# Performance work log

Hardware: AMD Instinct MI355X
Metric: run time of the kernel (lower is better)

Reference implementation:

```python
import jax, jax.numpy as jnp
import numpy as np

N, E = 50000, 800000
IN_CH, HID, OUT_CH = 128, 256, 40
L, R = 3, 16
EPS = 1e-12


def setup_inputs() -> dict:
    key = jax.random.key(0)
    ks = jax.random.split(key, 16)
    s = 0.05
    return {
        'x': jax.random.normal(ks[0], (N, IN_CH), jnp.float32),
        'edge_index': jax.random.randint(ks[1], (2, E), 0, N, dtype=jnp.int64),
        'W_in': jax.random.normal(ks[2], (IN_CH, HID), jnp.float32) * s,
        'b_in': jnp.zeros((HID,), jnp.float32),
        'centers': jax.random.normal(ks[3], (L, R, HID), jnp.float32),
        'log_sigma': jnp.zeros((L, R, HID), jnp.float32),
        'W_rule': jax.random.normal(ks[4], (L, R, HID, HID), jnp.float32) * s,
        'b_rule': jnp.zeros((L, R, HID), jnp.float32),
        'W_self': jax.random.normal(ks[5], (L, HID, HID), jnp.float32) * s,
        'b_self': jnp.zeros((L, HID), jnp.float32),
        'gamma': jnp.ones((L, HID), jnp.float32),
        'beta': jnp.zeros((L, HID), jnp.float32),
        'W_h1': jax.random.normal(ks[6], (HID, HID // 2), jnp.float32) * s,
        'b_h1': jnp.zeros((HID // 2,), jnp.float32),
        'W_h2': jax.random.normal(ks[7], (HID // 2, OUT_CH), jnp.float32) * s,
        'b_h2': jnp.zeros((OUT_CH,), jnp.float32),
    }


def membership(h, c, log_s):
    # Gaussian rule firing, expanded to matmuls to avoid [N,R,H] distance tensor
    inv_s2 = jnp.exp(-2.0 * log_s)                         # [R,H]
    d = (h * h) @ inv_s2.T - 2.0 * (h @ (c * inv_s2).T) \
        + jnp.sum(c * c * inv_s2, axis=-1)                 # [N,R]
    firing = jnp.exp(-0.5 * d)
    return firing / (jnp.sum(firing, axis=-1, keepdims=True) + EPS)


def fmpl(h, src, dst, c, log_s, W_r, b_r, W_s, b_s):
    n = h.shape[0]
    deg = jax.ops.segment_sum(jnp.ones(src.shape[0], h.dtype), dst, num_segments=n)
    agg = jax.ops.segment_sum(h[src], dst, num_segments=n) / jnp.clip(deg, 1.0)[:, None]
    mu = membership(h, c, log_s)                           # [N,R]
    per_rule = jnp.einsum('ni,rio->nro', agg, W_r) + b_r[None]  # [N,R,H]
    fuzzy = jnp.einsum('nr,nro->no', mu, per_rule)
    return h @ W_s + b_s + fuzzy


def batchnorm(x, g, b, eps=1e-5):
    m = jnp.mean(x, axis=0)
    v = jnp.var(x, axis=0)
    return (x - m) * jax.lax.rsqrt(v + eps) * g + b


def reference(x, edge_index, W_in, b_in, centers, log_sigma, W_rule, b_rule,
              W_self, b_self, gamma, beta, W_h1, b_h1, W_h2, b_h2):
    src, dst = edge_index[0], edge_index[1]
    h = jax.nn.relu(x @ W_in + b_in)                       # dropout = identity (eval)
    for l in range(L):
        h_new = fmpl(h, src, dst, centers[l], log_sigma[l], W_rule[l], b_rule[l],
                     W_self[l], b_self[l])
        h_new = jax.nn.relu(batchnorm(h_new, gamma[l], beta[l]))
        h = h + h_new
    logits = jax.nn.relu(h @ W_h1 + b_h1) @ W_h2 + b_h2
    return jax.nn.softmax(logits, axis=-1)
```

## Files before the change

kernel.cpp:

```cpp
#include <hip/hip_runtime.h>
#include <hip/hip_fp16.h>
#include <cstdint>
#include <cstddef>

using u16 = unsigned short;
using u32 = unsigned int;

typedef _Float16 half8 __attribute__((ext_vector_type(8)));
typedef float f32x4 __attribute__((ext_vector_type(4)));

static inline int cdiv(int a, int b) { return (a + b - 1) / b; }


__global__ void prep_k(const float* __restrict__ Wr,
                       const float* __restrict__ Ws, const float* __restrict__ br,
                       const float* __restrict__ W_in, const float* __restrict__ W_h1,
                       const float* __restrict__ W_h2,
                       const float* __restrict__ centers, const float* __restrict__ logsig,
                       u16* __restrict__ wcat,
                       u16* __restrict__ winp, u16* __restrict__ wh1p,
                       u16* __restrict__ wh2p,
                       u16* __restrict__ pcB, float* __restrict__ pccc,
                       int* __restrict__ zerobase, int nzero,
                       int Z, int Wb) {
    const int bid = blockIdx.x;
    const int tid = threadIdx.x;
    if (bid < Z) {
        int i = bid * 256 + tid;
        if (i < nzero) zerobase[i] = 0;
        return;
    }
    if (bid < Z + Wb) {
        size_t t = (size_t)(bid - Z) * 256 + tid;
        const size_t PL = 552u * 256u * 8u;
        int l = (int)(t / PL);
        size_t rem = t - (size_t)l * PL;
        int kp = (int)(rem >> 11);
        int o = (int)((rem >> 3) & 255);
        int e = (int)(rem & 7);
        int k = kp * 8 + e;
        float v;
        if (k < 4096)      v = Wr[((((size_t)l * 16 + (k >> 8)) * 256) + (k & 255)) * 256 + o];
        else if (k < 4352) v = Ws[(((size_t)l * 256) + (k - 4096)) * 256 + o];
        else if (k < 4368) v = br[(((size_t)l * 16) + (k - 4352)) * 256 + o];
        else               v = 0.f;
        union { u16 u; _Float16 h; } c; c.h = (_Float16)v;
        wcat[t] = c.u;
        return;
    }
    if (bid < Z + Wb + 128) {
        size_t t = (size_t)(bid - Z - Wb) * 256 + tid;
        int e = (int)(t & 7), o = (int)((t >> 3) & 255);
        int kp = (int)(t >> 11);
        union { u16 u; _Float16 h; } c; c.h = (_Float16)W_in[(size_t)(kp * 8 + e) * 256 + o];
        winp[t] = c.u;
        return;
    }
    if (bid < Z + Wb + 256) {
        size_t t = (size_t)(bid - Z - Wb - 128) * 256 + tid;
        int e = (int)(t & 7), o = (int)((t >> 3) & 127);
        int kp = (int)(t >> 10);
        union { u16 u; _Float16 h; } c; c.h = (_Float16)W_h1[(size_t)(kp * 8 + e) * 128 + o];
        wh1p[t] = c.u;
        return;
    }
    if (bid < Z + Wb + 256 + 24) {
        int t = (bid - Z - Wb - 256) * 256 + tid;
        int e = t & 7, col = (t >> 3) % 48, p = t / 384;
        int k = p * 8 + e;
        float v = (col < 40) ? W_h2[(size_t)k * 40 + col] : 0.f;
        union { u16 u; _Float16 h; } c; c.h = (_Float16)v;
        wh2p[t] = c.u;
        return;
    }
    {
        int lr = bid - (Z + Wb + 256 + 24);
        size_t idx = (size_t)lr * 256 + tid;
        float ls = logsig[idx];
        float inv = expf(-2.f * ls);
        float c = centers[idx];
        union { u16 u; _Float16 h; } c1, c2;
        c1.h = (_Float16)inv;
        c2.h = (_Float16)(-2.f * c * inv);
        pcB[(size_t)lr * 512 + tid] = c1.u;
        pcB[(size_t)lr * 512 + 256 + tid] = c2.u;
        __shared__ float sm[256];
        sm[tid] = c * c * inv;
        __syncthreads();
        for (int s = 128; s > 0; s >>= 1) { if (tid < s) sm[tid] += sm[tid + s]; __syncthreads(); }
        if (tid == 0) pccc[lr] = sm[0];
    }
}


__launch_bounds__(256, 4)
__global__ void csr_agg_g(const int* __restrict__ src, const int* __restrict__ dst,
                          int* __restrict__ deg, int* __restrict__ indptr,
                          int* __restrict__ cursor, float* __restrict__ deginv,
                          int* __restrict__ ssrc, int* __restrict__ csrctr,
                          const int* __restrict__ bflag, int* __restrict__ done,
                          const u16* __restrict__ h16, u16* __restrict__ agg16,
                          int E, int n) {
    if (bflag[511] == 0) return;
    const int tid = threadIdx.x;
    if (*done == 0) {
        auto gbar = [&](int id) {
            __threadfence();
            __syncthreads();
            if (tid == 0) {
                atomicAdd(csrctr, 1);
                while (atomicAdd(csrctr, 0) < 256 * id) __builtin_amdgcn_s_sleep(2);
            }
            __syncthreads();
        };
        for (int e = blockIdx.x * 256 + tid; e < E; e += 256 * 256)
            atomicAdd(&deg[dst[e]], 1);
        gbar(1);
        if (blockIdx.x == 0) {
            const int chunk = (n + 255) >> 8;
            int s0 = tid * chunk, s1 = s0 + chunk; if (s1 > n) s1 = n; if (s0 > n) s0 = n;
            int tot = 0;
            for (int i = s0; i < s1; ++i) tot += atomicAdd(&deg[i], 0);
            __shared__ int sm[256];
            sm[tid] = tot; __syncthreads();
            for (int off = 1; off < 256; off <<= 1) {
                int t = (tid >= off) ? sm[tid - off] : 0;
                __syncthreads(); sm[tid] += t; __syncthreads();
            }
            int base = sm[tid] - tot;
            for (int i = s0; i < s1; ++i) {
                int d = atomicAdd(&deg[i], 0);
                indptr[i] = base; cursor[i] = base;
                deginv[i] = 1.f / (float)(d > 1 ? d : 1);
                base += d;
            }
            if (tid == 255) indptr[n] = sm[255];
        }
        gbar(2);
        for (int e = blockIdx.x * 256 + tid; e < E; e += 256 * 256) {
            int d = dst[e];
            int pos = atomicAdd(&cursor[d], 1);
            ssrc[pos] = src[e];
        }
        gbar(3);
        if (blockIdx.x == 0 && tid == 0) *done = 1;
    }
    int lane = tid & 63, wave = tid >> 6;
    for (int node = blockIdx.x * 4 + wave; node < n; node += 256 * 4) {
        if (bflag[node >> 7] == 0) continue;
        int j0 = indptr[node], j1 = indptr[node + 1];
        float a0 = 0, a1 = 0, a2 = 0, a3 = 0;
        for (int j = j0; j < j1; ++j) {
            int sN = ssrc[j];
            union { uint2 u; _Float16 h[4]; } hv;
            hv.u = *(const uint2*)(h16 + (size_t)sN * 256 + lane * 4);
            a0 += (float)hv.h[0]; a1 += (float)hv.h[1];
            a2 += (float)hv.h[2]; a3 += (float)hv.h[3];
        }
        float di = deginv[node];
        union { uint2 u; _Float16 h[4]; } o;
        o.h[0] = (_Float16)(a0 * di); o.h[1] = (_Float16)(a1 * di);
        o.h[2] = (_Float16)(a2 * di); o.h[3] = (_Float16)(a3 * di);
        *(uint2*)(agg16 + (size_t)node * 256 + lane * 4) = o.u;
    }
}


__launch_bounds__(256)
__global__ void memb_k(const u16* __restrict__ h16, const u16* __restrict__ pcB,
                       const float* __restrict__ pccc,
                       u16* __restrict__ mu16, int* __restrict__ bflag, int n) {
    const int lane = threadIdx.x & 63, wave = threadIdx.x >> 6;
    const int q = lane >> 4, mm = lane & 15;
    const int n0 = (blockIdx.x * 4 + wave) * 16;
    if (n0 >= n) return;
    int nodeA = n0 + mm; if (nodeA >= n) nodeA = n - 1;
    const u16* hrow = h16 + (size_t)nodeA * 256;
    const u16* brow = pcB + (size_t)mm * 512;
    f32x4 acc = (f32x4){0.f, 0.f, 0.f, 0.f};
#pragma unroll
    for (int it = 0; it < 16; ++it) {
        int k = it * 32 + q * 8;
        half8 b = *(const half8*)(brow + k);
        half8 a;
        if (k < 256) {
            a = *(const half8*)(hrow + k);
            a = a * a;
        } else {
            a = *(const half8*)(hrow + (k - 256));
        }
        acc = __builtin_amdgcn_mfma_f32_16x16x32_f16(a, b, acc, 0, 0, 0);
    }
    float cc = pccc[mm];
    bool any = false;
#pragma unroll
    for (int r = 0; r < 4; ++r) {
        float d = acc[r] + cc;
        float f = expf(-0.5f * d);
        float s = f;
        s += __shfl_xor(s, 1); s += __shfl_xor(s, 2);
        s += __shfl_xor(s, 4); s += __shfl_xor(s, 8);
        int node = n0 + q * 4 + r;
        if (node < n) {
            union { u16 u; _Float16 h; } c2;
            c2.h = (_Float16)(f / (s + 1e-12f));
            mu16[(size_t)node * 16 + mm] = c2.u;
            if (c2.u != 0) any = true;
        }
    }
    if (__any(any) && lane == 0) {
        atomicOr(&bflag[n0 >> 7], 1);
        atomicOr(&bflag[511], 1);
    }
}


template <int MODE, int NCHUNK>
__launch_bounds__(256, 4)
__global__ void gemm_k(const u16* __restrict__ A, const u16* __restrict__ A2,
                       const u16* __restrict__ MU, const u16* __restrict__ Bp,
                       const float* __restrict__ bias, const int* __restrict__ bflag,
                       u16* __restrict__ outH, float* __restrict__ partial,
                       const u16* __restrict__ wh2, const float* __restrict__ bh2,
                       float* __restrict__ outF,
                       int nrows, int mcols, int astride) {
    __shared__ __align__(16) u16 lds[17408];
    __shared__ float bnbuf[512];
    u16* lA = lds;
    u16* lB = lds + 8192;
    const int tid = threadIdx.x;
    const int row0 = blockIdx.x * 128;
    const int c0 = blockIdx.y * 128;
    const int lane = tid & 63;
    const int q = lane >> 4, mm = lane & 15;
    const int wave = tid >> 6;
    const int wm = wave >> 1, wn = wave & 1;

    f32x4 acc[4][4];
#pragma unroll
    for (int i = 0; i < 4; ++i)
#pragma unroll
        for (int j = 0; j < 4; ++j) acc[i][j] = (f32x4){0.f, 0.f, 0.f, 0.f};

    int cb = 0, cbEnd = NCHUNK;
    if (MODE == 1 && bflag[blockIdx.x] == 0) { cb = 64; cbEnd = 68; }

    for (; cb < cbEnd; ++cb) {
#pragma unroll
        for (int it = 0; it < 4; ++it) {
            int idx = it * 256 + tid;
            int p = idx >> 7, col = idx & 127;
            uint4 v = *(const uint4*)(Bp + (((size_t)(cb * 8 + p)) * mcols + c0 + col) * 8);
            *(uint4*)(lB + (size_t)idx * 8) = v;
        }
#pragma unroll
        for (int it = 0; it < 4; ++it) {
            int idx = it * 256 + tid;
            int p = idx >> 7, row = idx & 127;
            int grow = row0 + row; if (grow >= nrows) grow = nrows - 1;
            uint4 v;
            if (MODE == 0) {
                const float* xr = (const float*)A + (size_t)grow * 128 + cb * 64 + (p << 3);
                float4 f0 = *(const float4*)xr;
                float4 f1 = *(const float4*)(xr + 4);
                union { uint4 u4; _Float16 h[8]; } cv;
                cv.h[0] = (_Float16)f0.x; cv.h[1] = (_Float16)f0.y;
                cv.h[2] = (_Float16)f0.z; cv.h[3] = (_Float16)f0.w;
                cv.h[4] = (_Float16)f1.x; cv.h[5] = (_Float16)f1.y;
                cv.h[6] = (_Float16)f1.z; cv.h[7] = (_Float16)f1.w;
                v = cv.u4;
            } else if (MODE == 2) {
                v = *(const uint4*)(A + (size_t)grow * astride + cb * 64 + p * 8);
            } else {
                if (cb < 64) {
                    int r = cb >> 2;
                    int i0 = ((cb & 3) << 6) + (p << 3);
                    v = *(const uint4*)(A + (size_t)grow * 256 + i0);
                    union { u16 u; _Float16 h; } mu; mu.u = MU[(size_t)grow * 16 + r];
                    union { uint4 u4; _Float16 h[8]; } wv; wv.u4 = v;
#pragma unroll
                    for (int j = 0; j < 8; ++j) wv.h[j] = wv.h[j] * mu.h;
                    v = wv.u4;
                } else if (cb < 68) {
                    int i0 = ((cb - 64) << 6) + (p << 3);
                    v = *(const uint4*)(A2 + (size_t)grow * 256 + i0);
                } else {
                    int j0 = p << 3;
                    if (j0 < 16) v = *(const uint4*)(MU + (size_t)grow * 16 + j0);
                    else v = (uint4){0, 0, 0, 0};
                }
            }
            *(uint4*)(lA + (size_t)idx * 8) = v;
        }
        __syncthreads();
#pragma unroll
        for (int kc = 0; kc < 2; ++kc) {
            int pp = kc * 4 + q;
            half8 af[4], bf[4];
#pragma unroll
            for (int mt = 0; mt < 4; ++mt)
                af[mt] = *(const half8*)(lA + ((size_t)pp * 128 + wm * 64 + mt * 16 + mm) * 8);
#pragma unroll
            for (int nt = 0; nt < 4; ++nt)
                bf[nt] = *(const half8*)(lB + ((size_t)pp * 128 + wn * 64 + nt * 16 + mm) * 8);
#pragma unroll
            for (int mt = 0; mt < 4; ++mt)
#pragma unroll
                for (int nt = 0; nt < 4; ++nt)
                    acc[mt][nt] = __builtin_amdgcn_mfma_f32_16x16x32_f16(af[mt], bf[nt], acc[mt][nt], 0, 0, 0);
        }
        __syncthreads();
    }

#pragma unroll
    for (int nt = 0; nt < 4; ++nt) {
        const int cl = wn * 64 + nt * 16 + mm;
        const int gcol = c0 + cl;
        float s = 0.f, ss = 0.f;
#pragma unroll
        for (int mt = 0; mt < 4; ++mt) {
#pragma unroll
            for (int r = 0; r < 4; ++r) {
                int row = wm * 64 + mt * 16 + q * 4 + r;
                float v = acc[mt][nt][r] + bias[gcol];
                if (MODE != 1) v = fmaxf(v, 0.f);
                union { u16 u; _Float16 h; } cc; cc.h = (_Float16)v;
                lds[row * 136 + cl] = cc.u;
                if (MODE == 1 && row0 + row < nrows) { s += v; ss += v * v; }
            }
        }
        if (MODE == 1) {
            s += __shfl_xor(s, 16);  s += __shfl_xor(s, 32);
            ss += __shfl_xor(ss, 16); ss += __shfl_xor(ss, 32);
            if (q == 0) {
                bnbuf[(wm * 128 + cl) * 2 + 0] = s;
                bnbuf[(wm * 128 + cl) * 2 + 1] = ss;
            }
        }
    }
    __syncthreads();

    if (MODE != 2) {
        int nr = nrows - row0; if (nr > 128) nr = 128;
#pragma unroll
        for (int it = 0; it < 8; ++it) {
            int idx = it * 256 + tid;
            int row = idx >> 4, cp = idx & 15;
            if (row < nr) {
                uint4 v = *(const uint4*)(lds + row * 136 + cp * 8);
                *(uint4*)(outH + (size_t)(row0 + row) * mcols + c0 + cp * 8) = v;
            }
        }
        if (MODE == 1) {
            int cl2 = tid >> 1, comp = tid & 1;
            float v = bnbuf[cl2 * 2 + comp] + bnbuf[(128 + cl2) * 2 + comp];
            partial[(size_t)blockIdx.x * 512 + comp * 256 + c0 + cl2] = v;
        }
    } else {
        const bool c2ok = (mm < 8);
        float b0 = bh2[mm], b1 = bh2[16 + mm];
        float b2 = c2ok ? bh2[32 + mm] : 0.f;
#pragma unroll
        for (int half = 0; half < 2; ++half) {
            int rbase = half * 64 + wave * 16;
            f32x4 hacc[3];
#pragma unroll
            for (int t = 0; t < 3; ++t) hacc[t] = (f32x4){0.f, 0.f, 0.f, 0.f};
#pragma unroll
            for (int c = 0; c < 4; ++c) {
                half8 a = *(const half8*)(lds + (rbase + mm) * 136 + c * 32 + q * 8);
#pragma unroll
                for (int t = 0; t < 3; ++t) {
                    half8 b = *(const half8*)(wh2 + ((size_t)(c * 4 + q) * 48 + t * 16 + mm) * 8);
                    hacc[t] = __builtin_amdgcn_mfma_f32_16x16x32_f16(a, b, hacc[t], 0, 0, 0);
                }
            }
#pragma unroll
            for (int r = 0; r < 4; ++r) {
                int node = row0 + rbase + q * 4 + r;
                float v0 = hacc[0][r] + b0;
                float v1 = hacc[1][r] + b1;
                float v2 = c2ok ? (hacc[2][r] + b2) : -3e38f;
                float m = fmaxf(fmaxf(v0, v1), v2);
                m = fmaxf(m, __shfl_xor(m, 1)); m = fmaxf(m, __shfl_xor(m, 2));
                m = fmaxf(m, __shfl_xor(m, 4)); m = fmaxf(m, __shfl_xor(m, 8));
                float e0 = expf(v0 - m), e1 = expf(v1 - m);
                float e2 = c2ok ? expf(v2 - m) : 0.f;
                float s = e0 + e1 + e2;
                s += __shfl_xor(s, 1); s += __shfl_xor(s, 2);
                s += __shfl_xor(s, 4); s += __shfl_xor(s, 8);
                float is = 1.f / s;
                if (node < nrows) {
                    float* op = outF + (size_t)node * 40;
                    op[mm] = e0 * is;
                    op[16 + mm] = e1 * is;
                    if (c2ok) op[32 + mm] = e2 * is;
                }
            }
        }
    }
}


__global__ void bnred_k(const float* __restrict__ partial, float* __restrict__ bnsum,
                        const float* __restrict__ gamma, const float* __restrict__ beta,
                        float* __restrict__ ab, int* __restrict__ bnctr, int n, int gx) {
    const int tid = threadIdx.x;
    const int g = blockIdx.x;
    float s = 0.f, qq = 0.f;
    for (int r = g; r < gx; r += 16) {
        s  += partial[(size_t)r * 512 + tid];
        qq += partial[(size_t)r * 512 + 256 + tid];
    }
    atomicAdd(&bnsum[tid], s);
    atomicAdd(&bnsum[256 + tid], qq);
    __threadfence();
    __shared__ int last;
    if (tid == 0) last = (atomicAdd(bnctr, 1) == 15);
    __syncthreads();
    if (!last) return;
    float su = atomicAdd(&bnsum[tid], 0.f);
    float sq = atomicAdd(&bnsum[256 + tid], 0.f);
    float invn = 1.f / (float)n;
    float m = su * invn;
    float al = gamma[tid] * rsqrtf(sq * invn - m * m + 1e-5f);
    ab[tid] = al;
    ab[256 + tid] = beta[tid] - m * al;
}


template <int DOMEMB>
__launch_bounds__(256)
__global__ void updmemb_k(const u16* __restrict__ pre16, const float* __restrict__ ab,
                          u16* __restrict__ h16,
                          const u16* __restrict__ pcB, const float* __restrict__ pccc,
                          u16* __restrict__ mu16, int* __restrict__ bflag, int n) {
    const int tid = threadIdx.x;
    const int lane = tid & 63, wave = tid >> 6;
    const int q = lane >> 4, mm = lane & 15;
    const int n0 = (blockIdx.x * 4 + wave) * 16;
    if (n0 >= n) return;
    const int node = n0 + mm;
    const bool valid = node < n;
    const int nodeC = valid ? node : n - 1;
    const size_t base = (size_t)nodeC * 256 + q * 8;

    half8 v16[8];
#pragma unroll
    for (int b = 0; b < 8; ++b) {
        int c = b * 32 + q * 8;
        float4 alA = *(const float4*)(ab + c);
        float4 alB = *(const float4*)(ab + c + 4);
        float4 shA = *(const float4*)(ab + 256 + c);
        float4 shB = *(const float4*)(ab + 256 + c + 4);
        float aarr[8] = {alA.x, alA.y, alA.z, alA.w, alB.x, alB.y, alB.z, alB.w};
        float harr[8] = {shA.x, shA.y, shA.z, shA.w, shB.x, shB.y, shB.z, shB.w};
        union { uint4 u; _Float16 hh[8]; } p, hv, o;
        p.u  = *(const uint4*)(pre16 + base + b * 32);
        hv.u = *(const uint4*)(h16 + base + b * 32);
#pragma unroll
        for (int j = 0; j < 8; ++j) {
            float v = (float)hv.hh[j] + fmaxf((float)p.hh[j] * aarr[j] + harr[j], 0.f);
            o.hh[j] = (_Float16)v;
        }
        if (valid) *(uint4*)(h16 + base + b * 32) = o.u;
        v16[b] = *(half8*)&o;
    }

    if (DOMEMB) {
        const u16* brow = pcB + (size_t)mm * 512;
        f32x4 acc = (f32x4){0.f, 0.f, 0.f, 0.f};
#pragma unroll
        for (int it = 0; it < 16; ++it) {
            half8 a = v16[it & 7];
            if (it < 8) a = a * a;
            half8 bb = *(const half8*)(brow + it * 32 + q * 8);
            acc = __builtin_amdgcn_mfma_f32_16x16x32_f16(a, bb, acc, 0, 0, 0);
        }
        float cc = pccc[mm];
        bool any = false;
#pragma unroll
        for (int r = 0; r < 4; ++r) {
            float d = acc[r] + cc;
            float f = expf(-0.5f * d);
            float s = f;
            s += __shfl_xor(s, 1); s += __shfl_xor(s, 2);
            s += __shfl_xor(s, 4); s += __shfl_xor(s, 8);
            int nd = n0 + q * 4 + r;
            if (nd < n) {
                union { u16 u; _Float16 h; } c2;
                c2.h = (_Float16)(f / (s + 1e-12f));
                mu16[(size_t)nd * 16 + mm] = c2.u;
                if (c2.u != 0) any = true;
            }
        }
        if (__any(any) && lane == 0) {
            atomicOr(&bflag[n0 >> 7], 1);
            atomicOr(&bflag[511], 1);
        }
    }
}


extern "C" void kernel_launch(void* const* d_in, const int* in_sizes, int n_in,
                              void* d_out, int out_size, void* d_ws, size_t ws_size,
                              hipStream_t stream) {
    const float* x       = (const float*)d_in[0];
    const int*   ei      = (const int*)d_in[1];
    const float* W_in    = (const float*)d_in[2];
    const float* b_in    = (const float*)d_in[3];
    const float* centers = (const float*)d_in[4];
    const float* logsig  = (const float*)d_in[5];
    const float* W_rule  = (const float*)d_in[6];
    const float* b_rule  = (const float*)d_in[7];
    const float* W_self  = (const float*)d_in[8];
    const float* b_self  = (const float*)d_in[9];
    const float* gamma   = (const float*)d_in[10];
    const float* beta    = (const float*)d_in[11];
    const float* W_h1    = (const float*)d_in[12];
    const float* b_h1    = (const float*)d_in[13];
    const float* W_h2    = (const float*)d_in[14];
    const float* b_h2    = (const float*)d_in[15];

    const int N = in_sizes[0] / 128;
    const int E = in_sizes[1] / 2;
    const int* e_src = ei;
    const int* e_dst = ei + E;

    char* w = (char*)d_ws;
    size_t off = 0;
    auto alloc = [&](size_t bytes) -> void* {
        void* p = w + off;
        off = (off + bytes + 255) & ~(size_t)255;
        return p;
    };

    const int gx = cdiv(N, 128);

    u16*   h16    = (u16*)  alloc((size_t)N * 256 * 2);
    u16*   pre16  = (u16*)  alloc((size_t)N * 256 * 2);
    u16*   agg16  = (u16*)  alloc((size_t)N * 256 * 2);
    u16*   mu16   = (u16*)  alloc((size_t)N * 16 * 2);
    u16*   wcat   = (u16*)  alloc((size_t)3 * 552 * 256 * 8 * 2);
    u16*   winp   = (u16*)  alloc((size_t)16 * 256 * 8 * 2);
    u16*   wh1p   = (u16*)  alloc((size_t)32 * 128 * 8 * 2);
    u16*   wh2p   = (u16*)  alloc((size_t)16 * 48 * 8 * 2);
    u16*   pcB    = (u16*)  alloc((size_t)48 * 512 * 2);
    float* pccc   = (float*)alloc((size_t)48 * 4);
    int*   indptr = (int*)  alloc((size_t)(N + 1) * 4);
    int*   cursor = (int*)  alloc((size_t)N * 4);
    float* deginv = (float*)alloc((size_t)N * 4);
    int*   ssrc   = (int*)  alloc((size_t)E * 4);
    float* partial= (float*)alloc((size_t)gx * 512 * 4);
    float* abA    = (float*)alloc((size_t)3 * 512 * 4);
    const int nzero = N + 3 * 512 + 3 * 512 + 16;
    int*   zerob  = (int*)  alloc((size_t)nzero * 4);
    int*   deg    = zerob;
    int*   bflagA = zerob + N;
    float* bnsumA = (float*)(zerob + N + 3 * 512);
    int*   misc   = zerob + N + 3 * 512 + 3 * 512;
    int*   done   = misc;
    int*   csrctr = misc + 1;
    int*   bnctr  = misc + 2;

    const int Z = cdiv(nzero, 256);
    const int Wb = 3 * 552 * 256 * 8 / 256;
    const int prep_grid = Z + Wb + 128 + 128 + 24 + 48;

    prep_k<<<prep_grid, 256, 0, stream>>>(W_rule, W_self, b_rule, W_in, W_h1, W_h2,
                                          centers, logsig, wcat, winp, wh1p, wh2p,
                                          pcB, pccc, zerob, nzero, Z, Wb);

    gemm_k<0, 2><<<dim3(gx, 2), 256, 0, stream>>>((const u16*)x, nullptr, nullptr, winp,
                                                  b_in, nullptr, h16, nullptr, nullptr,
                                                  nullptr, nullptr, N, 256, 128);
    memb_k<<<cdiv(N, 64), 256, 0, stream>>>(h16, pcB, pccc, mu16, bflagA, N);

    for (int l = 0; l < 3; ++l) {
        int* bf = bflagA + l * 512;
        float* bns = bnsumA + l * 512;
        float* ab = abA + l * 512;
        csr_agg_g<<<256, 256, 0, stream>>>(e_src, e_dst, deg, indptr, cursor, deginv,
                                           ssrc, csrctr, bf, done, h16, agg16, E, N);
        gemm_k<1, 69><<<dim3(gx, 2), 256, 0, stream>>>(agg16, h16, mu16,
                                                       wcat + (size_t)l * 552 * 256 * 8,
                                                       b_self + l * 256, bf, pre16,
                                                       partial, nullptr, nullptr, nullptr,
                                                       N, 256, 0);
        bnred_k<<<16, 256, 0, stream>>>(partial, bns, gamma + l * 256, beta + l * 256,
                                        ab, bnctr + l, N, gx);
        if (l < 2) {
            updmemb_k<1><<<cdiv(N, 64), 256, 0, stream>>>(pre16, ab, h16,
                                                          pcB + (size_t)(l + 1) * 16 * 512,
                                                          pccc + (l + 1) * 16, mu16,
                                                          bflagA + (l + 1) * 512, N);
        } else {
            updmemb_k<0><<<cdiv(N, 64), 256, 0, stream>>>(pre16, ab, h16,
                                                          nullptr, nullptr, nullptr,
                                                          nullptr, N);
        }
    }

    gemm_k<2, 4><<<dim3(gx, 1), 256, 0, stream>>>(h16, nullptr, nullptr, wh1p, b_h1,
                                                  nullptr, nullptr, nullptr, wh2p, b_h2,
                                                  (float*)d_out, N, 128, 256);
}
```

Baseline: 337.1 us.

## Use full-width GEMM tiles, fuse membership into input GEMM and drop BN reduction kernel

The main GEMM now computes all 256 output columns per 128-row block instead of splitting columns across two blocks. Each block loads the A tile (the mu-scaled aggregation) once rather than twice, at the cost of more accumulator registers and lower occupancy (launch bounds 2). The input GEMM also computes the first-layer membership in its epilogue, which removes the separate memb_k launch and a re-read of h. The batchnorm column sums are atomically accumulated directly from the GEMM, and alpha/shift are recomputed in updmemb_k, which eliminates the bnred_k launch. The head GEMM is split into its own kernel.

```diff
diff --git a/kernel.cpp b/kernel.cpp
--- a/kernel.cpp
+++ b/kernel.cpp
@@ -166,91 +166,40 @@
 }
 
 
-__launch_bounds__(256)
-__global__ void memb_k(const u16* __restrict__ h16, const u16* __restrict__ pcB,
-                       const float* __restrict__ pccc,
-                       u16* __restrict__ mu16, int* __restrict__ bflag, int n) {
-    const int lane = threadIdx.x & 63, wave = threadIdx.x >> 6;
-    const int q = lane >> 4, mm = lane & 15;
-    const int n0 = (blockIdx.x * 4 + wave) * 16;
-    if (n0 >= n) return;
-    int nodeA = n0 + mm; if (nodeA >= n) nodeA = n - 1;
-    const u16* hrow = h16 + (size_t)nodeA * 256;
-    const u16* brow = pcB + (size_t)mm * 512;
-    f32x4 acc = (f32x4){0.f, 0.f, 0.f, 0.f};
-#pragma unroll
-    for (int it = 0; it < 16; ++it) {
-        int k = it * 32 + q * 8;
-        half8 b = *(const half8*)(brow + k);
-        half8 a;
-        if (k < 256) {
-            a = *(const half8*)(hrow + k);
-            a = a * a;
-        } else {
-            a = *(const half8*)(hrow + (k - 256));
-        }
-        acc = __builtin_amdgcn_mfma_f32_16x16x32_f16(a, b, acc, 0, 0, 0);
-    }
-    float cc = pccc[mm];
-    bool any = false;
-#pragma unroll
-    for (int r = 0; r < 4; ++r) {
-        float d = acc[r] + cc;
-        float f = expf(-0.5f * d);
-        float s = f;
-        s += __shfl_xor(s, 1); s += __shfl_xor(s, 2);
-        s += __shfl_xor(s, 4); s += __shfl_xor(s, 8);
-        int node = n0 + q * 4 + r;
-        if (node < n) {
-            union { u16 u; _Float16 h; } c2;
-            c2.h = (_Float16)(f / (s + 1e-12f));
-            mu16[(size_t)node * 16 + mm] = c2.u;
-            if (c2.u != 0) any = true;
-        }
-    }
-    if (__any(any) && lane == 0) {
-        atomicOr(&bflag[n0 >> 7], 1);
-        atomicOr(&bflag[511], 1);
-    }
-}
-
-
 template <int MODE, int NCHUNK>
-__launch_bounds__(256, 4)
-__global__ void gemm_k(const u16* __restrict__ A, const u16* __restrict__ A2,
-                       const u16* __restrict__ MU, const u16* __restrict__ Bp,
-                       const float* __restrict__ bias, const int* __restrict__ bflag,
-                       u16* __restrict__ outH, float* __restrict__ partial,
-                       const u16* __restrict__ wh2, const float* __restrict__ bh2,
-                       float* __restrict__ outF,
-                       int nrows, int mcols, int astride) {
-    __shared__ __align__(16) u16 lds[17408];
-    __shared__ float bnbuf[512];
+__launch_bounds__(256, 2)
+__global__ void gemm_mn(const u16* __restrict__ A, const u16* __restrict__ A2,
+                        const u16* __restrict__ MU, const u16* __restrict__ Bp,
+                        const float* __restrict__ bias, const int* __restrict__ bflag,
+                        u16* __restrict__ outH, float* __restrict__ bnsum,
+                        const u16* __restrict__ pcB, const float* __restrict__ pccc,
+                        u16* __restrict__ mu16, int* __restrict__ bflagN,
+                        int nrows) {
+    __shared__ __align__(16) u16 lds[24576];
+    __shared__ float bnbuf[2048];
     u16* lA = lds;
     u16* lB = lds + 8192;
     const int tid = threadIdx.x;
     const int row0 = blockIdx.x * 128;
-    const int c0 = blockIdx.y * 128;
     const int lane = tid & 63;
     const int q = lane >> 4, mm = lane & 15;
     const int wave = tid >> 6;
-    const int wm = wave >> 1, wn = wave & 1;
-
-    f32x4 acc[4][4];
-#pragma unroll
-    for (int i = 0; i < 4; ++i)
-#pragma unroll
-        for (int j = 0; j < 4; ++j) acc[i][j] = (f32x4){0.f, 0.f, 0.f, 0.f};
+
+    f32x4 acc[2][16];
+#pragma unroll
+    for (int i = 0; i < 2; ++i)
+#pragma unroll
+        for (int j = 0; j < 16; ++j) acc[i][j] = (f32x4){0.f, 0.f, 0.f, 0.f};
 
     int cb = 0, cbEnd = NCHUNK;
     if (MODE == 1 && bflag[blockIdx.x] == 0) { cb = 64; cbEnd = 68; }
 
     for (; cb < cbEnd; ++cb) {
 #pragma unroll
-        for (int it = 0; it < 4; ++it) {
+        for (int it = 0; it < 8; ++it) {
             int idx = it * 256 + tid;
-            int p = idx >> 7, col = idx & 127;
-            uint4 v = *(const uint4*)(Bp + (((size_t)(cb * 8 + p)) * mcols + c0 + col) * 8);
+            int p = idx >> 8, col = idx & 255;
+            uint4 v = *(const uint4*)(Bp + (((size_t)(cb * 8 + p)) * 256 + col) * 8);
             *(uint4*)(lB + (size_t)idx * 8) = v;
         }
 #pragma unroll
@@ -269,8 +218,6 @@
                 cv.h[4] = (_Float16)f1.x; cv.h[5] = (_Float16)f1.y;
                 cv.h[6] = (_Float16)f1.z; cv.h[7] = (_Float16)f1.w;
                 v = cv.u4;
-            } else if (MODE == 2) {
-                v = *(const uint4*)(A + (size_t)grow * astride + cb * 64 + p * 8);
             } else {
                 if (cb < 64) {
                     int r = cb >> 2;
@@ -296,146 +243,151 @@
 #pragma unroll
         for (int kc = 0; kc < 2; ++kc) {
             int pp = kc * 4 + q;
-            half8 af[4], bf[4];
-#pragma unroll
-            for (int mt = 0; mt < 4; ++mt)
-                af[mt] = *(const half8*)(lA + ((size_t)pp * 128 + wm * 64 + mt * 16 + mm) * 8);
-#pragma unroll
-            for (int nt = 0; nt < 4; ++nt)
-                bf[nt] = *(const half8*)(lB + ((size_t)pp * 128 + wn * 64 + nt * 16 + mm) * 8);
-#pragma unroll
-            for (int mt = 0; mt < 4; ++mt)
-#pragma unroll
-                for (int nt = 0; nt < 4; ++nt)
-                    acc[mt][nt] = __builtin_amdgcn_mfma_f32_16x16x32_f16(af[mt], bf[nt], acc[mt][nt], 0, 0, 0);
-        }
-        __syncthreads();
-    }
-
-#pragma unroll
-    for (int nt = 0; nt < 4; ++nt) {
-        const int cl = wn * 64 + nt * 16 + mm;
-        const int gcol = c0 + cl;
-        float s = 0.f, ss = 0.f;
-#pragma unroll
-        for (int mt = 0; mt < 4; ++mt) {
-#pragma unroll
-            for (int r = 0; r < 4; ++r) {
-                int row = wm * 64 + mt * 16 + q * 4 + r;
-                float v = acc[mt][nt][r] + bias[gcol];
-                if (MODE != 1) v = fmaxf(v, 0.f);
-                union { u16 u; _Float16 h; } cc; cc.h = (_Float16)v;
-                lds[row * 136 + cl] = cc.u;
-                if (MODE == 1 && row0 + row < nrows) { s += v; ss += v * v; }
-            }
-        }
-        if (MODE == 1) {
+            half8 af0 = *(const half8*)(lA + ((size_t)pp * 128 + wave * 32 + mm) * 8);
+            half8 af1 = *(const half8*)(lA + ((size_t)pp * 128 + wave * 32 + 16 + mm) * 8);
+#pragma unroll
+            for (int nt = 0; nt < 16; ++nt) {
+                half8 bf = *(const half8*)(lB + ((size_t)pp * 256 + nt * 16 + mm) * 8);
+                acc[0][nt] = __builtin_amdgcn_mfma_f32_16x16x32_f16(af0, bf, acc[0][nt], 0, 0, 0);
+                acc[1][nt] = __builtin_amdgcn_mfma_f32_16x16x32_f16(af1, bf, acc[1][nt], 0, 0, 0);
+            }
+        }
+        __syncthreads();
+    }
+
+    int nr = nrows - row0; if (nr > 128) nr = 128;
+
+    if (MODE == 1) {
+#pragma unroll
+        for (int nt = 0; nt < 16; ++nt) {
+            int cl = nt * 16 + mm;
+            float bb = bias[cl];
+            float s = 0.f, ss = 0.f;
+#pragma unroll
+            for (int mt = 0; mt < 2; ++mt) {
+#pragma unroll
+                for (int r = 0; r < 4; ++r) {
+                    int row = wave * 32 + mt * 16 + q * 4 + r;
+                    float v = acc[mt][nt][r] + bb;
+                    if (row < nr) { s += v; ss += v * v; }
+                }
+            }
             s += __shfl_xor(s, 16);  s += __shfl_xor(s, 32);
             ss += __shfl_xor(ss, 16); ss += __shfl_xor(ss, 32);
             if (q == 0) {
-                bnbuf[(wm * 128 + cl) * 2 + 0] = s;
-                bnbuf[(wm * 128 + cl) * 2 + 1] = ss;
-            }
-        }
-    }
-    __syncthreads();
-
-    if (MODE != 2) {
-        int nr = nrows - row0; if (nr > 128) nr = 128;
+                bnbuf[(wave * 256 + cl) * 2 + 0] = s;
+                bnbuf[(wave * 256 + cl) * 2 + 1] = ss;
+            }
+        }
+        __syncthreads();
+        {
+            float s  = bnbuf[tid * 2]     + bnbuf[(256 + tid) * 2]
+                     + bnbuf[(512 + tid) * 2] + bnbuf[(768 + tid) * 2];
+            float ss = bnbuf[tid * 2 + 1] + bnbuf[(256 + tid) * 2 + 1]
+                     + bnbuf[(512 + tid) * 2 + 1] + bnbuf[(768 + tid) * 2 + 1];
+            atomicAdd(&bnsum[tid], s);
+            atomicAdd(&bnsum[256 + tid], ss);
+        }
+    }
+
+    f32x4 macc0 = (f32x4){0.f, 0.f, 0.f, 0.f};
+    f32x4 macc1 = (f32x4){0.f, 0.f, 0.f, 0.f};
+#pragma unroll
+    for (int h = 0; h < 2; ++h) {
+        __syncthreads();
+#pragma unroll
+        for (int nt = 0; nt < 8; ++nt) {
+            int cl = h * 128 + nt * 16 + mm;
+            float bb = bias[cl];
+#pragma unroll
+            for (int mt = 0; mt < 2; ++mt) {
+#pragma unroll
+                for (int r = 0; r < 4; ++r) {
+                    int row = wave * 32 + mt * 16 + q * 4 + r;
+                    float v = acc[mt][h * 8 + nt][r] + bb;
+                    if (MODE == 0) v = fmaxf(v, 0.f);
+                    union { u16 u; _Float16 hh; } cc; cc.hh = (_Float16)v;
+                    lds[row * 136 + nt * 16 + mm] = cc.u;
+                }
+            }
+        }
+        __syncthreads();
 #pragma unroll
         for (int it = 0; it < 8; ++it) {
             int idx = it * 256 + tid;
             int row = idx >> 4, cp = idx & 15;
             if (row < nr) {
                 uint4 v = *(const uint4*)(lds + row * 136 + cp * 8);
-                *(uint4*)(outH + (size_t)(row0 + row) * mcols + c0 + cp * 8) = v;
-            }
-        }
-        if (MODE == 1) {
-            int cl2 = tid >> 1, comp = tid & 1;
-            float v = bnbuf[cl2 * 2 + comp] + bnbuf[(128 + cl2) * 2 + comp];
-            partial[(size_t)blockIdx.x * 512 + comp * 256 + c0 + cl2] = v;
-        }
-    } else {
-        const bool c2ok = (mm < 8);
-        float b0 = bh2[mm], b1 = bh2[16 + mm];
-        float b2 = c2ok ? bh2[32 + mm] : 0.f;
-#pragma unroll
-        for (int half = 0; half < 2; ++half) {
-            int rbase = half * 64 + wave * 16;
-            f32x4 hacc[3];
-#pragma unroll
-            for (int t = 0; t < 3; ++t) hacc[t] = (f32x4){0.f, 0.f, 0.f, 0.f};
-#pragma unroll
-            for (int c = 0; c < 4; ++c) {
-                half8 a = *(const half8*)(lds + (rbase + mm) * 136 + c * 32 + q * 8);
-#pragma unroll
-                for (int t = 0; t < 3; ++t) {
-                    half8 b = *(const half8*)(wh2 + ((size_t)(c * 4 + q) * 48 + t * 16 + mm) * 8);
-                    hacc[t] = __builtin_amdgcn_mfma_f32_16x16x32_f16(a, b, hacc[t], 0, 0, 0);
-                }
-            }
+                *(uint4*)(outH + (size_t)(row0 + row) * 256 + h * 128 + cp * 8) = v;
+            }
+        }
+        if (MODE == 0) {
+            const u16* brow = pcB + (size_t)mm * 512;
+#pragma unroll
+            for (int it2 = 0; it2 < 4; ++it2) {
+                int lk = it2 * 32 + q * 8;
+                half8 b1 = *(const half8*)(brow + h * 128 + lk);
+                half8 b2 = *(const half8*)(brow + 256 + h * 128 + lk);
+                half8 a0 = *(const half8*)(lds + ((size_t)(wave * 32 + mm)) * 136 + lk);
+                half8 a1 = *(const half8*)(lds + ((size_t)(wave * 32 + 16 + mm)) * 136 + lk);
+                macc0 = __builtin_amdgcn_mfma_f32_16x16x32_f16(a0 * a0, b1, macc0, 0, 0, 0);
+                macc0 = __builtin_amdgcn_mfma_f32_16x16x32_f16(a0, b2, macc0, 0, 0, 0);
+                macc1 = __builtin_amdgcn_mfma_f32_16x16x32_f16(a1 * a1, b1, macc1, 0, 0, 0);
+                macc1 = __builtin_amdgcn_mfma_f32_16x16x32_f16(a1, b2, macc1, 0, 0, 0);
+            }
+        }
+    }
+
+    if (MODE == 0) {
+        float cc = pccc[mm];
+        bool any = false;
+#pragma unroll
+        for (int g = 0; g < 2; ++g) {
+            f32x4 macc = g ? macc1 : macc0;
 #pragma unroll
             for (int r = 0; r < 4; ++r) {
-                int node = row0 + rbase + q * 4 + r;
-                float v0 = hacc[0][r] + b0;
-                float v1 = hacc[1][r] + b1;
-                float v2 = c2ok ? (hacc[2][r] + b2) : -3e38f;
-                float m = fmaxf(fmaxf(v0, v1), v2);
-                m = fmaxf(m, __shfl_xor(m, 1)); m = fmaxf(m, __shfl_xor(m, 2));
-                m = fmaxf(m, __shfl_xor(m, 4)); m = fmaxf(m, __shfl_xor(m, 8));
-                float e0 = expf(v0 - m), e1 = expf(v1 - m);
-                float e2 = c2ok ? expf(v2 - m) : 0.f;
-                float s = e0 + e1 + e2;
+                float d = macc[r] + cc;
+                float f = expf(-0.5f * d);
+                float s = f;
                 s += __shfl_xor(s, 1); s += __shfl_xor(s, 2);
                 s += __shfl_xor(s, 4); s += __shfl_xor(s, 8);
-                float is = 1.f / s;
+                int node = row0 + (wave * 2 + g) * 16 + q * 4 + r;
                 if (node < nrows) {
-                    float* op = outF + (size_t)node * 40;
-                    op[mm] = e0 * is;
-                    op[16 + mm] = e1 * is;
-                    if (c2ok) op[32 + mm] = e2 * is;
+                    union { u16 u; _Float16 hh; } c2;
+                    c2.hh = (_Float16)(f / (s + 1e-12f));
+                    mu16[(size_t)node * 16 + mm] = c2.u;
+                    if (c2.u != 0) any = true;
                 }
             }
         }
-    }
-}
-
-
-__global__ void bnred_k(const float* __restrict__ partial, float* __restrict__ bnsum,
-                        const float* __restrict__ gamma, const float* __restrict__ beta,
-                        float* __restrict__ ab, int* __restrict__ bnctr, int n, int gx) {
-    const int tid = threadIdx.x;
-    const int g = blockIdx.x;
-    float s = 0.f, qq = 0.f;
-    for (int r = g; r < gx; r += 16) {
-        s  += partial[(size_t)r * 512 + tid];
-        qq += partial[(size_t)r * 512 + 256 + tid];
-    }
-    atomicAdd(&bnsum[tid], s);
-    atomicAdd(&bnsum[256 + tid], qq);
-    __threadfence();
-    __shared__ int last;
-    if (tid == 0) last = (atomicAdd(bnctr, 1) == 15);
-    __syncthreads();
-    if (!last) return;
-    float su = atomicAdd(&bnsum[tid], 0.f);
-    float sq = atomicAdd(&bnsum[256 + tid], 0.f);
-    float invn = 1.f / (float)n;
-    float m = su * invn;
-    float al = gamma[tid] * rsqrtf(sq * invn - m * m + 1e-5f);
-    ab[tid] = al;
-    ab[256 + tid] = beta[tid] - m * al;
+        if (__any(any) && lane == 0) {
+            atomicOr(&bflagN[blockIdx.x], 1);
+            atomicOr(&bflagN[511], 1);
+        }
+    }
 }
 
 
 template <int DOMEMB>
 __launch_bounds__(256)
-__global__ void updmemb_k(const u16* __restrict__ pre16, const float* __restrict__ ab,
+__global__ void updmemb_k(const u16* __restrict__ pre16, const float* __restrict__ bnsum,
+                          const float* __restrict__ gamma, const float* __restrict__ beta,
                           u16* __restrict__ h16,
                           const u16* __restrict__ pcB, const float* __restrict__ pccc,
                           u16* __restrict__ mu16, int* __restrict__ bflag, int n) {
     const int tid = threadIdx.x;
+    __shared__ float l_ab[512];
+    {
+        float su = bnsum[tid];
+        float sq = bnsum[256 + tid];
+        float invn = 1.f / (float)n;
+        float m = su * invn;
+        float al = gamma[tid] * rsqrtf(sq * invn - m * m + 1e-5f);
+        l_ab[tid] = al;
+        l_ab[256 + tid] = beta[tid] - m * al;
+    }
+    __syncthreads();
+
     const int lane = tid & 63, wave = tid >> 6;
     const int q = lane >> 4, mm = lane & 15;
     const int n0 = (blockIdx.x * 4 + wave) * 16;
@@ -449,10 +401,10 @@
 #pragma unroll
     for (int b = 0; b < 8; ++b) {
         int c = b * 32 + q * 8;
-        float4 alA = *(const float4*)(ab + c);
-        float4 alB = *(const float4*)(ab + c + 4);
-        float4 shA = *(const float4*)(ab + 256 + c);
-        float4 shB = *(const float4*)(ab + 256 + c + 4);
+        float4 alA = *(const float4*)(l_ab + c);
+        float4 alB = *(const float4*)(l_ab + c + 4);
+        float4 shA = *(const float4*)(l_ab + 256 + c);
+        float4 shB = *(const float4*)(l_ab + 256 + c + 4);
         float aarr[8] = {alA.x, alA.y, alA.z, alA.w, alB.x, alB.y, alB.z, alB.w};
         float harr[8] = {shA.x, shA.y, shA.z, shA.w, shB.x, shB.y, shB.z, shB.w};
         union { uint4 u; _Float16 hh[8]; } p, hv, o;
@@ -497,6 +449,123 @@
         if (__any(any) && lane == 0) {
             atomicOr(&bflag[n0 >> 7], 1);
             atomicOr(&bflag[511], 1);
+        }
+    }
+}
+
+
+__launch_bounds__(256, 4)
+__global__ void head_k(const u16* __restrict__ A, const u16* __restrict__ Bp,
+                       const float* __restrict__ bias,
+                       const u16* __restrict__ wh2, const float* __restrict__ bh2,
+                       float* __restrict__ outF, int nrows) {
+    __shared__ __align__(16) u16 lds[17408];
+    u16* lA = lds;
+    u16* lB = lds + 8192;
+    const int tid = threadIdx.x;
+    const int row0 = blockIdx.x * 128;
+    const int lane = tid & 63;
+    const int q = lane >> 4, mm = lane & 15;
+    const int wave = tid >> 6;
+    const int wm = wave >> 1, wn = wave & 1;
+
+    f32x4 acc[4][4];
+#pragma unroll
+    for (int i = 0; i < 4; ++i)
+#pragma unroll
+        for (int j = 0; j < 4; ++j) acc[i][j] = (f32x4){0.f, 0.f, 0.f, 0.f};
+
+    for (int cb = 0; cb < 4; ++cb) {
+#pragma unroll
+        for (int it = 0; it < 4; ++it) {
+            int idx = it * 256 + tid;
+            int p = idx >> 7, col = idx & 127;
+            uint4 v = *(const uint4*)(Bp + (((size_t)(cb * 8 + p)) * 128 + col) * 8);
+            *(uint4*)(lB + (size_t)idx * 8) = v;
+        }
+#pragma unroll
+        for (int it = 0; it < 4; ++it) {
+            int idx = it * 256 + tid;
+            int p = idx >> 7, row = idx & 127;
+            int grow = row0 + row; if (grow >= nrows) grow = nrows - 1;
+            uint4 v = *(const uint4*)(A + (size_t)grow * 256 + cb * 64 + p * 8);
+            *(uint4*)(lA + (size_t)idx * 8) = v;
+        }
+        __syncthreads();
+#pragma unroll
+        for (int kc = 0; kc < 2; ++kc) {
+            int pp = kc * 4 + q;
+            half8 af[4], bf[4];
+#pragma unroll
+            for (int mt = 0; mt < 4; ++mt)
+                af[mt] = *(const half8*)(lA + ((size_t)pp * 128 + wm * 64 + mt * 16 + mm) * 8);
+#pragma unroll
+            for (int nt = 0; nt < 4; ++nt)
+                bf[nt] = *(const half8*)(lB + ((size_t)pp * 128 + wn * 64 + nt * 16 + mm) * 8);
+#pragma unroll
+            for (int mt = 0; mt < 4; ++mt)
+#pragma unroll
+                for (int nt = 0; nt < 4; ++nt)
+                    acc[mt][nt] = __builtin_amdgcn_mfma_f32_16x16x32_f16(af[mt], bf[nt], acc[mt][nt], 0, 0, 0);
+        }
+        __syncthreads();
+    }
+
+#pragma unroll
+    for (int nt = 0; nt < 4; ++nt) {
+        const int cl = wn * 64 + nt * 16 + mm;
+#pragma unroll
+        for (int mt = 0; mt < 4; ++mt) {
+#pragma unroll
+            for (int r = 0; r < 4; ++r) {
+                int row = wm * 64 + mt * 16 + q * 4 + r;
+                float v = fmaxf(acc[mt][nt][r] + bias[cl], 0.f);
+                union { u16 u; _Float16 h; } cc; cc.h = (_Float16)v;
+                lds[row * 136 + cl] = cc.u;
+            }
+        }
+    }
+    __syncthreads();
+
+    const bool c2ok = (mm < 8);
+    float b0 = bh2[mm], b1 = bh2[16 + mm];
+    float b2 = c2ok ? bh2[32 + mm] : 0.f;
+#pragma unroll
+    for (int half = 0; half < 2; ++half) {
+        int rbase = half * 64 + wave * 16;
+        f32x4 hacc[3];
+#pragma unroll
+        for (int t = 0; t < 3; ++t) hacc[t] = (f32x4){0.f, 0.f, 0.f, 0.f};
+#pragma unroll
+        for (int c = 0; c < 4; ++c) {
+            half8 a = *(const half8*)(lds + (rbase + mm) * 136 + c * 32 + q * 8);
+#pragma unroll
+            for (int t = 0; t < 3; ++t) {
+                half8 b = *(const half8*)(wh2 + ((size_t)(c * 4 + q) * 48 + t * 16 + mm) * 8);
+                hacc[t] = __builtin_amdgcn_mfma_f32_16x16x32_f16(a, b, hacc[t], 0, 0, 0);
+            }
+        }
+#pragma unroll
+        for (int r = 0; r < 4; ++r) {
+            int node = row0 + rbase + q * 4 + r;
+            float v0 = hacc[0][r] + b0;
+            float v1 = hacc[1][r] + b1;
+            float v2 = c2ok ? (hacc[2][r] + b2) : -3e38f;
+            float m = fmaxf(fmaxf(v0, v1), v2);
+            m = fmaxf(m, __shfl_xor(m, 1)); m = fmaxf(m, __shfl_xor(m, 2));
+            m = fmaxf(m, __shfl_xor(m, 4)); m = fmaxf(m, __shfl_xor(m, 8));
+            float e0 = expf(v0 - m), e1 = expf(v1 - m);
+            float e2 = c2ok ? expf(v2 - m) : 0.f;
+            float s = e0 + e1 + e2;
+            s += __shfl_xor(s, 1); s += __shfl_xor(s, 2);
+            s += __shfl_xor(s, 4); s += __shfl_xor(s, 8);
+            float is = 1.f / s;
+            if (node < nrows) {
+                float* op = outF + (size_t)node * 40;
+                op[mm] = e0 * is;
+                op[16 + mm] = e1 * is;
+                if (c2ok) op[32 + mm] = e2 * is;
+            }
         }
     }
 }
@@ -551,8 +620,6 @@
     int*   cursor = (int*)  alloc((size_t)N * 4);
     float* deginv = (float*)alloc((size_t)N * 4);
     int*   ssrc   = (int*)  alloc((size_t)E * 4);
-    float* partial= (float*)alloc((size_t)gx * 512 * 4);
-    float* abA    = (float*)alloc((size_t)3 * 512 * 4);
     const int nzero = N + 3 * 512 + 3 * 512 + 16;
     int*   zerob  = (int*)  alloc((size_t)nzero * 4);
     int*   deg    = zerob;
@@ -561,7 +628,6 @@
     int*   misc   = zerob + N + 3 * 512 + 3 * 512;
     int*   done   = misc;
     int*   csrctr = misc + 1;
-    int*   bnctr  = misc + 2;
 
     const int Z = cdiv(nzero, 256);
     const int Wb = 3 * 552 * 256 * 8 / 256;
@@ -571,37 +637,32 @@
                                           centers, logsig, wcat, winp, wh1p, wh2p,
                                           pcB, pccc, zerob, nzero, Z, Wb);
 
-    gemm_k<0, 2><<<dim3(gx, 2), 256, 0, stream>>>((const u16*)x, nullptr, nullptr, winp,
-                                                  b_in, nullptr, h16, nullptr, nullptr,
-                                                  nullptr, nullptr, N, 256, 128);
-    memb_k<<<cdiv(N, 64), 256, 0, stream>>>(h16, pcB, pccc, mu16, bflagA, N);
+    gemm_mn<0, 2><<<gx, 256, 0, stream>>>((const u16*)x, nullptr, nullptr, winp,
+                                          b_in, nullptr, h16, nullptr,
+                                          pcB, pccc, mu16, bflagA, N);
 
     for (int l = 0; l < 3; ++l) {
         int* bf = bflagA + l * 512;
         float* bns = bnsumA + l * 512;
-        float* ab = abA + l * 512;
         csr_agg_g<<<256, 256, 0, stream>>>(e_src, e_dst, deg, indptr, cursor, deginv,
                                            ssrc, csrctr, bf, done, h16, agg16, E, N);
-        gemm_k<1, 69><<<dim3(gx, 2), 256, 0, stream>>>(agg16, h16, mu16,
-                                                       wcat + (size_t)l * 552 * 256 * 8,
-                                                       b_self + l * 256, bf, pre16,
-                                                       partial, nullptr, nullptr, nullptr,
-                                                       N, 256, 0);
-        bnred_k<<<16, 256, 0, stream>>>(partial, bns, gamma + l * 256, beta + l * 256,
-                                        ab, bnctr + l, N, gx);
+        gemm_mn<1, 69><<<gx, 256, 0, stream>>>(agg16, h16, mu16,
+                                               wcat + (size_t)l * 552 * 256 * 8,
+                                               b_self + l * 256, bf, pre16, bns,
+                                               nullptr, nullptr, nullptr, nullptr, N);
         if (l < 2) {
-            updmemb_k<1><<<cdiv(N, 64), 256, 0, stream>>>(pre16, ab, h16,
+            updmemb_k<1><<<cdiv(N, 64), 256, 0, stream>>>(pre16, bns, gamma + l * 256,
+                                                          beta + l * 256, h16,
                                                           pcB + (size_t)(l + 1) * 16 * 512,
                                                           pccc + (l + 1) * 16, mu16,
                                                           bflagA + (l + 1) * 512, N);
         } else {
-            updmemb_k<0><<<cdiv(N, 64), 256, 0, stream>>>(pre16, ab, h16,
+            updmemb_k<0><<<cdiv(N, 64), 256, 0, stream>>>(pre16, bns, gamma + l * 256,
+                                                          beta + l * 256, h16,
                                                           nullptr, nullptr, nullptr,
                                                           nullptr, N);
         }
     }
 
-    gemm_k<2, 4><<<dim3(gx, 1), 256, 0, stream>>>(h16, nullptr, nullptr, wh1p, b_h1,
-                                                  nullptr, nullptr, nullptr, wh2p, b_h2,
-                                                  (float*)d_out, N, 128, 256);
+    head_k<<<gx, 256, 0, stream>>>(h16, wh1p, b_h1, wh2p, b_h2, (float*)d_out, N);
 }
```

Result: faster. 310.3 us (-8.0%).
